# Kernel tuning notes

Hardware: AMD Instinct MI355X
Metric: run time of the kernel (lower is better)

## Reference

```python
import jax, jax.numpy as jnp
import numpy as np

NP, NM = 50, 32          # pathways, misc tokens
T = NP + NM              # 82 total tokens
D = 24                   # token_dim for latent_dim=2048: (2048//82)//4*4
H, DH, FF = 4, 6, 96     # heads, head_dim, ffn dim (4*D)
B = 8192
EPS = 1e-5


def _ln(x, g, b):
    m = x.mean(-1, keepdims=True)
    v = ((x - m) ** 2).mean(-1, keepdims=True)
    return (x - m) / jnp.sqrt(v + EPS) * g + b


def _adapter(x, w1, b1, g1, bb1, w2, b2, g2, bb2, w3, b3):
    # Linear -> LN -> GELU -> (Dropout eval) -> Linear -> LN -> GELU -> Linear
    h = jax.nn.gelu(_ln(x @ w1.T + b1, g1, bb1), approximate=False)
    h = jax.nn.gelu(_ln(h @ w2.T + b2, g2, bb2), approximate=False)
    return h @ w3.T + b3


def _enc_layer(x, wqkv, bqkv, wo, bo, lg1, lb1, fw1, fb1, fw2, fb2, lg2, lb2):
    # post-norm TransformerEncoderLayer (PyTorch defaults: relu FFN, batch_first)
    Bx, Tx, Dx = x.shape
    qkv = x @ wqkv.T + bqkv                       # [B,T,3D]
    q, k, v = jnp.split(qkv, 3, axis=-1)
    sh = lambda a: a.reshape(Bx, Tx, H, DH).transpose(0, 2, 1, 3)
    q, k, v = sh(q), sh(k), sh(v)
    att = jax.nn.softmax(jnp.einsum('bhqd,bhkd->bhqk', q, k) / jnp.sqrt(jnp.float32(DH)), axis=-1)
    o = jnp.einsum('bhqk,bhkd->bhqd', att, v).transpose(0, 2, 1, 3).reshape(Bx, Tx, Dx)
    o = o @ wo.T + bo
    x = _ln(x + o, lg1, lb1)
    f = jax.nn.relu(x @ fw1.T + fb1) @ fw2.T + fb2
    return _ln(x + f, lg2, lb2)


def setup_inputs() -> dict:
    key = jax.random.key(0)
    ks = iter(jax.random.split(key, 40))
    r = lambda *s: jax.random.normal(next(ks), s, dtype=jnp.float32) * 0.02
    inp = {
        'gene': jax.random.normal(next(ks), (B, 5000), dtype=jnp.float32),
        'protein': jax.random.normal(next(ks), (B, 226), dtype=jnp.float32),
        'pathway_tokens': jax.random.normal(next(ks), (NP, D), dtype=jnp.float32),
        'misc_tokens': jax.random.normal(next(ks), (NM, D), dtype=jnp.float32),
        # gene adapter: 5000 -> 512 -> 256 -> 82
        'gw1': r(512, 5000), 'gb1': jnp.zeros(512), 'gg1': jnp.ones(512), 'gbb1': jnp.zeros(512),
        'gw2': r(256, 512), 'gb2': jnp.zeros(256), 'gg2': jnp.ones(256), 'gbb2': jnp.zeros(256),
        'gw3': r(T, 256), 'gb3': jnp.zeros(T),
        # protein adapter: 226 -> 512 -> 256 -> 82
        'pw1': r(512, 226), 'pb1': jnp.zeros(512), 'pg1': jnp.ones(512), 'pbb1': jnp.zeros(512),
        'pw2': r(256, 512), 'pb2': jnp.zeros(256), 'pg2': jnp.ones(256), 'pbb2': jnp.zeros(256),
        'pw3': r(T, 256), 'pb3': jnp.zeros(T),
        # token mixer: 2 stacked TransformerEncoder layers
        'wqkv': r(2, 3 * D, D), 'bqkv': jnp.zeros((2, 3 * D)),
        'wo': r(2, D, D), 'bo': jnp.zeros((2, D)),
        'lg1': jnp.ones((2, D)), 'lb1': jnp.zeros((2, D)),
        'fw1': r(2, FF, D), 'fb1': jnp.zeros((2, FF)),
        'fw2': r(2, D, FF), 'fb2': jnp.zeros((2, D)),
        'lg2': jnp.ones((2, D)), 'lb2': jnp.zeros((2, D)),
    }
    return inp


def reference(gene, protein, pathway_tokens, misc_tokens,
              gw1, gb1, gg1, gbb1, gw2, gb2, gg2, gbb2, gw3, gb3,
              pw1, pb1, pg1, pbb1, pw2, pb2, pg2, pbb2, pw3, pb3,
              wqkv, bqkv, wo, bo, lg1, lb1, fw1, fb1, fw2, fb2, lg2, lb2):
    all_tokens = jnp.concatenate([pathway_tokens, misc_tokens], axis=0)    # [T,D]
    gene_w = jax.nn.softmax(_adapter(gene, gw1, gb1, gg1, gbb1, gw2, gb2, gg2, gbb2, gw3, gb3), axis=-1)
    prot_w = jax.nn.softmax(_adapter(protein, pw1, pb1, pg1, pbb1, pw2, pb2, pg2, pbb2, pw3, pb3), axis=-1)
    # vectorized form of the per-batch loop: token_activations[b] += all_tokens * w[b,:,None]
    acts = (gene_w + prot_w)[:, :, None] * all_tokens[None]               # [B,T,D]
    for l in range(2):
        acts = _enc_layer(acts, wqkv[l], bqkv[l], wo[l], bo[l], lg1[l], lb1[l],
                          fw1[l], fb1[l], fw2[l], fb2[l], lg2[l], lb2[l])
    return acts
```

## Files before the change

### kernel.cpp

```cpp
#include <hip/hip_runtime.h>
#include <hip/hip_bf16.h>
#include <math.h>

typedef __attribute__((ext_vector_type(4))) float f32x4;
typedef __attribute__((ext_vector_type(8))) short s16x8;
typedef __attribute__((ext_vector_type(4))) short s16x4;
typedef __attribute__((ext_vector_type(4))) unsigned int u32x4;
typedef __attribute__((ext_vector_type(2))) unsigned int u32x2;
typedef _Float16 h2 __attribute__((ext_vector_type(2)));

static __device__ __forceinline__ unsigned short f2bf(float f) {
  unsigned int u = __builtin_bit_cast(unsigned int, f);
  u += 0x7FFFu + ((u >> 16) & 1u);
  return (unsigned short)(u >> 16);
}
static __device__ __forceinline__ unsigned int pk2bf(float a, float b) {
  return (unsigned int)f2bf(a) | ((unsigned int)f2bf(b) << 16);
}
static __device__ __forceinline__ float gelu_exact(float x) {
  return 0.5f * x * (1.0f + erff(x * 0.7071067811865475f));
}
static __device__ __forceinline__ h2 pkh2(float a, float b) {
#if __has_builtin(__builtin_amdgcn_cvt_pkrtz)
  return __builtin_bit_cast(h2, __builtin_amdgcn_cvt_pkrtz(a, b));
#else
  h2 r; r[0] = (_Float16)a; r[1] = (_Float16)b; return r;
#endif
}
static __device__ __forceinline__ float dot2u(h2 a, unsigned int b, float c) {
  h2 bh = __builtin_bit_cast(h2, b);
#if __has_builtin(__builtin_amdgcn_fdot2)
  return __builtin_amdgcn_fdot2(a, bh, c, false);
#else
  return fmaf((float)a[0], (float)bh[0], fmaf((float)a[1], (float)bh[1], c));
#endif
}
static __device__ __forceinline__ float exp2fast(float x) {
#if __has_builtin(__builtin_amdgcn_exp2f)
  return __builtin_amdgcn_exp2f(x);
#else
  return exp2f(x);
#endif
}
static __device__ __forceinline__ void gll16(const void* g, void* l) {
#if __has_builtin(__builtin_amdgcn_global_load_lds)
  __builtin_amdgcn_global_load_lds((__attribute__((address_space(1))) void*)(void*)g,
                                   (__attribute__((address_space(3))) void*)l, 16, 0, 0);
#else
  *(u32x4*)l = *(const u32x4*)g;
#endif
}


__global__ __launch_bounds__(256)
void convert_tile_kernel(const float* __restrict__ src, unsigned short* __restrict__ dst,
                         int Msrc, int Ksrc, int TK, int total16) {
  const int id = blockIdx.x * 256 + threadIdx.x;
  if (id >= total16) return;
  const int j = id & 511;
  const int tile = id >> 9;
  const int tk = tile % TK;
  const int tmm = tile / TK;
  const int r = j >> 3, cb = j & 7;
  const int lcb = cb ^ (r & 7);
  const int row = tmm * 64 + r;
  const int col = tk * 64 + lcb * 8;
  float v[8];
  #pragma unroll
  for (int i = 0; i < 8; ++i) v[i] = 0.f;
  if (row < Msrc) {
    const size_t base = (size_t)row * Ksrc + col;
    if (col + 8 <= Ksrc && ((base & 3) == 0)) {
      f32x4 a = *(const f32x4*)(src + base);
      f32x4 b = *(const f32x4*)(src + base + 4);
      v[0]=a[0];v[1]=a[1];v[2]=a[2];v[3]=a[3];
      v[4]=b[0];v[5]=b[1];v[6]=b[2];v[7]=b[3];
    } else {
      #pragma unroll
      for (int i = 0; i < 8; ++i) if (col + i < Ksrc) v[i] = src[base + i];
    }
  }
  u32x4 o = { pk2bf(v[0],v[1]), pk2bf(v[2],v[3]), pk2bf(v[4],v[5]), pk2bf(v[6],v[7]) };
  *(u32x4*)(dst + (size_t)id * 8) = o;
}

__global__ __launch_bounds__(256, 4)
void gemm_bf16t_kernel(const unsigned short* __restrict__ At, const unsigned short* __restrict__ Bt,
                       const float* __restrict__ bias, float* __restrict__ C,
                       int NT, int KT, int Ntrue, int Nld) {
  __shared__ unsigned short As[4096];
  __shared__ unsigned short Bs[8192];
  const int tid = threadIdx.x;
  const int lane = tid & 63;
  const int wid = tid >> 6;
  const int wm = wid >> 1, wn = wid & 1;
  const int lr = lane & 15;
  const int lkb = ((lane >> 4) & 3) * 16;
  const int l = blockIdx.x;
  const int xcd = l & 7;
  const int kl = l >> 3;
  const int nb = kl % NT;
  const int tm = (kl / NT) * 8 + xcd;
  const size_t abase = (size_t)tm * KT * 4096;
  const size_t bbase0 = (size_t)(2 * nb) * KT * 4096;
  const size_t bbase1 = (size_t)(2 * nb + 1) * KT * 4096;

  f32x4 acc[2][4];
  #pragma unroll
  for (int m = 0; m < 2; ++m)
    #pragma unroll
    for (int n = 0; n < 4; ++n) acc[m][n] = (f32x4){0.f,0.f,0.f,0.f};

  for (int tk = 0; tk < KT; ++tk) {
    __syncthreads();
    const unsigned short* at = At + abase + (size_t)tk * 4096;
    const unsigned short* b0 = Bt + bbase0 + (size_t)tk * 4096;
    const unsigned short* b1 = Bt + bbase1 + (size_t)tk * 4096;
    gll16(at + tid * 8,        (char*)As + tid * 16);
    gll16(at + 2048 + tid * 8, (char*)As + 4096 + tid * 16);
    gll16(b0 + tid * 8,        (char*)Bs + tid * 16);
    gll16(b0 + 2048 + tid * 8, (char*)Bs + 4096 + tid * 16);
    gll16(b1 + tid * 8,        (char*)Bs + 8192 + tid * 16);
    gll16(b1 + 2048 + tid * 8, (char*)Bs + 12288 + tid * 16);
    __syncthreads();
    #pragma unroll
    for (int kk = 0; kk < 2; ++kk) {
      const int kb = (kk * 64 + lkb) ^ ((lr & 7) << 4);
      s16x8 af[2], bfr[4];
      #pragma unroll
      for (int m = 0; m < 2; ++m) {
        const int r = wm * 32 + m * 16 + lr;
        af[m] = *(const s16x8*)((const char*)As + r * 128 + kb);
      }
      #pragma unroll
      for (int n = 0; n < 4; ++n) {
        const int c = wn * 64 + n * 16 + lr;
        bfr[n] = *(const s16x8*)((const char*)Bs + (c >> 6) * 8192 + (c & 63) * 128 + kb);
      }
      #pragma unroll
      for (int m = 0; m < 2; ++m)
        #pragma unroll
        for (int n = 0; n < 4; ++n)
          acc[m][n] = __builtin_amdgcn_mfma_f32_16x16x32_bf16(af[m], bfr[n], acc[m][n], 0, 0, 0);
    }
  }
  const int crow = (lane >> 4) * 4;
  #pragma unroll
  for (int m = 0; m < 2; ++m) {
    const int row = tm * 64 + wm * 32 + m * 16 + crow;
    #pragma unroll
    for (int n = 0; n < 4; ++n) {
      const int col = nb * 128 + wn * 64 + n * 16 + lr;
      if (col < Ntrue) {
        const float bv = bias[col];
        #pragma unroll
        for (int i = 0; i < 4; ++i)
          C[(size_t)(row + i) * Nld + col] = acc[m][n][i] + bv;
      }
    }
  }
}

__global__ __launch_bounds__(256)
void ln_gelu_b16t_kernel(const float* __restrict__ X, const float* __restrict__ g,
                         const float* __restrict__ bta, unsigned short* __restrict__ Y,
                         int N, int TK) {
  const int lane = threadIdx.x & 63;
  const int row = blockIdx.x * 4 + (threadIdx.x >> 6);
  const int tmv = row >> 6, r = row & 63;
  const float* xr = X + (size_t)row * N;
  if (N == 512) {
    const int c0 = lane * 8;
    f32x4 a = *(const f32x4*)(xr + c0);
    f32x4 b = *(const f32x4*)(xr + c0 + 4);
    float s = a[0]+a[1]+a[2]+a[3]+b[0]+b[1]+b[2]+b[3];
    float ss = a[0]*a[0]+a[1]*a[1]+a[2]*a[2]+a[3]*a[3]+b[0]*b[0]+b[1]*b[1]+b[2]*b[2]+b[3]*b[3];
    #pragma unroll
    for (int off = 1; off < 64; off <<= 1) { s += __shfl_xor(s, off); ss += __shfl_xor(ss, off); }
    const float mean = s * (1.f/512.f);
    const float var = ss * (1.f/512.f) - mean * mean;
    const float rstd = rsqrtf(var + 1e-5f);
    float z[8];
    #pragma unroll
    for (int i = 0; i < 4; ++i) z[i]   = gelu_exact((a[i]-mean)*rstd*g[c0+i]   + bta[c0+i]);
    #pragma unroll
    for (int i = 0; i < 4; ++i) z[4+i] = gelu_exact((b[i]-mean)*rstd*g[c0+4+i] + bta[c0+4+i]);
    const int tk = lane >> 3, lcb = lane & 7;
    const size_t d16 = ((size_t)(tmv * TK + tk) << 9) + (r << 3) + (lcb ^ (r & 7));
    u32x4 o = { pk2bf(z[0],z[1]), pk2bf(z[2],z[3]), pk2bf(z[4],z[5]), pk2bf(z[6],z[7]) };
    *(u32x4*)(Y + d16 * 8) = o;
  } else {
    const int c0 = lane * 4;
    f32x4 a = *(const f32x4*)(xr + c0);
    float s = a[0]+a[1]+a[2]+a[3];
    float ss = a[0]*a[0]+a[1]*a[1]+a[2]*a[2]+a[3]*a[3];
    #pragma unroll
    for (int off = 1; off < 64; off <<= 1) { s += __shfl_xor(s, off); ss += __shfl_xor(ss, off); }
    const float mean = s * (1.f/256.f);
    const float var = ss * (1.f/256.f) - mean * mean;
    const float rstd = rsqrtf(var + 1e-5f);
    float z[4];
    #pragma unroll
    for (int i = 0; i < 4; ++i) z[i] = gelu_exact((a[i]-mean)*rstd*g[c0+i] + bta[c0+i]);
    const int tk = lane >> 4, lcb = (lane >> 1) & 7, half = lane & 1;
    const size_t d16 = ((size_t)(tmv * TK + tk) << 9) + (r << 3) + (lcb ^ (r & 7));
    u32x2 o = { pk2bf(z[0],z[1]), pk2bf(z[2],z[3]) };
    *(u32x2*)(Y + d16 * 8 + half * 4) = o;
  }
}

#define GBM 64
#define GBN 128
#define GBK 64
#define GLDS 72

__global__ __launch_bounds__(256, 2)
void gemm_bias_kernel(const float* __restrict__ A, const float* __restrict__ Bw,
                      const float* __restrict__ bias, float* __restrict__ C,
                      int M, int N, int K) {
  __shared__ short As[GBM * GLDS];
  __shared__ short Bs[GBN * GLDS];
  const int tid = threadIdx.x;
  const int lane = tid & 63;
  const int wid = tid >> 6;
  const int wm = wid >> 1;
  const int wn = wid & 1;
  const int m0 = blockIdx.x * GBM;
  const int n0 = blockIdx.y * GBN;
  const int lr = lane & 15;
  const int lk = (lane >> 4) * 8;
  const bool kAligned = ((K & 3) == 0);
  f32x4 acc[2][4];
  #pragma unroll
  for (int i = 0; i < 2; ++i)
    #pragma unroll
    for (int j = 0; j < 4; ++j) acc[i][j] = (f32x4){0.f, 0.f, 0.f, 0.f};
  for (int k0 = 0; k0 < K; k0 += GBK) {
    __syncthreads();
    const bool fullK = kAligned && (k0 + GBK <= K);
    #pragma unroll
    for (int pass = 0; pass < 4; ++pass) {
      const int f = pass * 1024 + tid * 4;
      const int r = f >> 6, c = f & 63;
      f32x4 v = (f32x4){0.f, 0.f, 0.f, 0.f};
      const float* src = A + (size_t)(m0 + r) * K + (k0 + c);
      if (fullK) v = *(const f32x4*)src;
      else {
        #pragma unroll
        for (int i = 0; i < 4; ++i) if (k0 + c + i < K) v[i] = src[i];
      }
      s16x4 sv = { (short)f2bf(v[0]), (short)f2bf(v[1]), (short)f2bf(v[2]), (short)f2bf(v[3]) };
      *(s16x4*)&As[r * GLDS + c] = sv;
    }
    #pragma unroll
    for (int pass = 0; pass < 8; ++pass) {
      const int f = pass * 1024 + tid * 4;
      const int r = f >> 6, c = f & 63;
      f32x4 v = (f32x4){0.f, 0.f, 0.f, 0.f};
      if (n0 + r < N) {
        const float* src = Bw + (size_t)(n0 + r) * K + (k0 + c);
        if (fullK) v = *(const f32x4*)src;
        else {
          #pragma unroll
          for (int i = 0; i < 4; ++i) if (k0 + c + i < K) v[i] = src[i];
        }
      }
      s16x4 sv = { (short)f2bf(v[0]), (short)f2bf(v[1]), (short)f2bf(v[2]), (short)f2bf(v[3]) };
      *(s16x4*)&Bs[r * GLDS + c] = sv;
    }
    __syncthreads();
    #pragma unroll
    for (int kk = 0; kk < GBK; kk += 32) {
      s16x8 af[2], bfr[4];
      #pragma unroll
      for (int m = 0; m < 2; ++m)
        af[m] = *(const s16x8*)&As[(wm * 32 + m * 16 + lr) * GLDS + kk + lk];
      #pragma unroll
      for (int n = 0; n < 4; ++n)
        bfr[n] = *(const s16x8*)&Bs[(wn * 64 + n * 16 + lr) * GLDS + kk + lk];
      #pragma unroll
      for (int m = 0; m < 2; ++m)
        #pragma unroll
        for (int n = 0; n < 4; ++n)
          acc[m][n] = __builtin_amdgcn_mfma_f32_16x16x32_bf16(af[m], bfr[n], acc[m][n], 0, 0, 0);
    }
  }
  const int crow = (lane >> 4) * 4;
  #pragma unroll
  for (int m = 0; m < 2; ++m) {
    const int row = m0 + wm * 32 + m * 16 + crow;
    #pragma unroll
    for (int n = 0; n < 4; ++n) {
      const int col = n0 + wn * 64 + n * 16 + lr;
      if (col < N) {
        const float bv = bias[col];
        #pragma unroll
        for (int i = 0; i < 4; ++i)
          C[(size_t)(row + i) * N + col] = acc[m][n][i] + bv;
      }
    }
  }
}

__global__ __launch_bounds__(256)
void ln_gelu_kernel(const float* __restrict__ X, const float* __restrict__ g,
                    const float* __restrict__ bta, float* __restrict__ Y, int N) {
  const int row = blockIdx.x;
  const float* xr = X + (size_t)row * N;
  float* yr = Y + (size_t)row * N;
  const int tid = threadIdx.x;
  const float e0 = xr[tid];
  float e1 = 0.f;
  const bool two = (N > 256);
  if (two) e1 = xr[tid + 256];
  float s = e0 + e1;
  float ss = e0 * e0 + e1 * e1;
  #pragma unroll
  for (int off = 1; off < 64; off <<= 1) { s += __shfl_xor(s, off); ss += __shfl_xor(ss, off); }
  __shared__ float red[8];
  const int w = tid >> 6;
  if ((tid & 63) == 0) { red[w] = s; red[4 + w] = ss; }
  __syncthreads();
  s  = red[0] + red[1] + red[2] + red[3];
  ss = red[4] + red[5] + red[6] + red[7];
  const float invN = 1.0f / (float)N;
  const float mean = s * invN;
  const float var = ss * invN - mean * mean;
  const float rstd = rsqrtf(var + 1e-5f);
  { const float z = (e0 - mean) * rstd * g[tid] + bta[tid]; yr[tid] = gelu_exact(z); }
  if (two) { const float z = (e1 - mean) * rstd * g[tid + 256] + bta[tid + 256]; yr[tid + 256] = gelu_exact(z); }
}

__global__ __launch_bounds__(256)
void softmax2_kernel(const float* __restrict__ la, const float* __restrict__ lp,
                     float* __restrict__ w, int B) {
  const int wid = threadIdx.x >> 6;
  const int lane = threadIdx.x & 63;
  const int row = blockIdx.x * 4 + wid;
  if (row >= B) return;
  const bool has2 = (lane < 18);
  const float* a = la + (size_t)row * 82;
  const float* p = lp + (size_t)row * 82;
  float a0 = a[lane], a1 = has2 ? a[64 + lane] : -1e30f;
  float m = fmaxf(a0, a1);
  #pragma unroll
  for (int off = 1; off < 64; off <<= 1) m = fmaxf(m, __shfl_xor(m, off));
  float ea0 = __expf(a0 - m);
  float ea1 = has2 ? __expf(a1 - m) : 0.f;
  float sa = ea0 + ea1;
  #pragma unroll
  for (int off = 1; off < 64; off <<= 1) sa += __shfl_xor(sa, off);
  float p0 = p[lane], p1 = has2 ? p[64 + lane] : -1e30f;
  float mp = fmaxf(p0, p1);
  #pragma unroll
  for (int off = 1; off < 64; off <<= 1) mp = fmaxf(mp, __shfl_xor(mp, off));
  float ep0 = __expf(p0 - mp);
  float ep1 = has2 ? __expf(p1 - mp) : 0.f;
  float sp = ep0 + ep1;
  #pragma unroll
  for (int off = 1; off < 64; off <<= 1) sp += __shfl_xor(sp, off);
  const float ia = 1.0f / sa, ip = 1.0f / sp;
  w[(size_t)row * 82 + lane] = ea0 * ia + ep0 * ip;
  if (has2) w[(size_t)row * 82 + 64 + lane] = ea1 * ia + ep1 * ip;
}

__global__ __launch_bounds__(256)
void pack_weights_kernel(const float* __restrict__ wqkv, const float* __restrict__ wo,
                         const float* __restrict__ fw1, const float* __restrict__ fw2,
                         unsigned int* __restrict__ dst) {
  const int i = blockIdx.x * 256 + threadIdx.x;
  if (i >= 6912) return;
  float a, b;
  if (i < 1728)      { a = wqkv[2 * i];            b = wqkv[2 * i + 1]; }
  else if (i < 2304) { int j = i - 1728; a = wo[2 * j];  b = wo[2 * j + 1]; }
  else if (i < 4608) { int j = i - 2304; a = fw1[2 * j]; b = fw1[2 * j + 1]; }
  else {
    int j = i - 4608; int layer = j / 1152; int r = j % 1152;
    int jp = r / 24; int d = r % 24;
    const float* s = fw2 + layer * 2304 + d * 96 + 2 * jp;
    a = s[0]; b = s[1];
  }
  unsigned short lo = __builtin_bit_cast(unsigned short, (_Float16)a);
  unsigned short hi = __builtin_bit_cast(unsigned short, (_Float16)b);
  dst[i] = (unsigned int)lo | ((unsigned int)hi << 16);
}

#define VSTRIDE 28

__global__ __launch_bounds__(256, 4)
void encoder_kernel(const float* __restrict__ w_sum,
                    const float* __restrict__ pathway, const float* __restrict__ misc,
                    const unsigned int* __restrict__ whb,
                    const float* __restrict__ bqkv, const float* __restrict__ bo,
                    const float* __restrict__ lg1, const float* __restrict__ lb1,
                    const float* __restrict__ fb1, const float* __restrict__ fb2,
                    const float* __restrict__ lg2, const float* __restrict__ lb2,
                    float* __restrict__ out, int Btot) {
  __shared__ unsigned int Ks[247 * 12];
  __shared__ unsigned int Vs[124 * VSTRIDE];
  const int tid = threadIdx.x;
  const bool active = (tid < 246);
  const int rowW = active ? tid : 246;
  int ls = tid / 82; if (ls > 2) ls = 2;
  const int t = active ? (tid - ls * 82) : 0;
  const int vrow = active ? (ls * 41 + (t >> 1)) : 123;
  const int b = blockIdx.x * 3 + ls;
  const bool storeOK = active && (b < Btot);
  const int bb = (b < Btot) ? b : (Btot - 1);
  float x[24];
  {
    const float* trow = (t < 50) ? (pathway + t * 24) : (misc + (t - 50) * 24);
    const float wv = w_sum[(size_t)bb * 82 + t];
    #pragma unroll
    for (int i = 0; i < 6; ++i) {
      f32x4 v = *(const f32x4*)(trow + 4 * i);
      x[4*i+0] = wv * v[0]; x[4*i+1] = wv * v[1];
      x[4*i+2] = wv * v[2]; x[4*i+3] = wv * v[3];
    }
  }
  const float QS = 0.5889777913f;
  float xf[24];
  #pragma unroll 1
  for (int layer = 0; layer < 2; ++layer) {
    const unsigned int* Wqh = whb + layer * 864;
    const unsigned int* Woh = whb + 1728 + layer * 288;
    const unsigned int* F1h = whb + 2304 + layer * 1152;
    const unsigned int* F2t = whb + 4608 + layer * 1152;
    const float* Bq = bqkv + layer * 72;
    h2 xh[12];
    #pragma unroll
    for (int i = 0; i < 12; ++i) xh[i] = pkh2(x[2*i], x[2*i+1]);
    h2 qh[12];
    #pragma unroll
    for (int j2 = 0; j2 < 12; ++j2) {
      float s0 = Bq[2*j2], s1 = Bq[2*j2+1];
      const unsigned int* w0 = Wqh + (2*j2) * 12;
      #pragma unroll
      for (int kd = 0; kd < 12; ++kd) { s0 = dot2u(xh[kd], w0[kd], s0); s1 = dot2u(xh[kd], w0[12 + kd], s1); }
      qh[j2] = pkh2(s0 * QS, s1 * QS);
    }
    {
      unsigned int kpk[12];
      #pragma unroll
      for (int j2 = 0; j2 < 12; ++j2) {
        float s0 = Bq[24 + 2*j2], s1 = Bq[25 + 2*j2];
        const unsigned int* w0 = Wqh + (24 + 2*j2) * 12;
        #pragma unroll
        for (int kd = 0; kd < 12; ++kd) { s0 = dot2u(xh[kd], w0[kd], s0); s1 = dot2u(xh[kd], w0[12 + kd], s1); }
        kpk[j2] = __builtin_bit_cast(unsigned int, pkh2(s0, s1));
      }
      #pragma unroll
      for (int u = 0; u < 3; ++u)
        *(u32x4*)&Ks[rowW * 12 + 4*u] = (u32x4){kpk[4*u], kpk[4*u+1], kpk[4*u+2], kpk[4*u+3]};
      float vv[24];
      #pragma unroll
      for (int j2 = 0; j2 < 12; ++j2) {
        float s0 = Bq[48 + 2*j2], s1 = Bq[49 + 2*j2];
        const unsigned int* w0 = Wqh + (48 + 2*j2) * 12;
        #pragma unroll
        for (int kd = 0; kd < 12; ++kd) { s0 = dot2u(xh[kd], w0[kd], s0); s1 = dot2u(xh[kd], w0[12 + kd], s1); }
        vv[2*j2] = s0; vv[2*j2+1] = s1;
      }
      _Float16* vh = (_Float16*)Vs;
      const int vbase = vrow * (2 * VSTRIDE) + (t & 1);
      #pragma unroll
      for (int j = 0; j < 24; ++j) vh[vbase + 2*j] = (_Float16)vv[j];
    }
    __syncthreads();
    float acc_o[24];
    float lsum[4] = {0.f, 0.f, 0.f, 0.f};
    #pragma unroll
// ... 88 lines not shown
      float sa = Bf1[2*jp], sb = Bf1[2*jp+1];
      const unsigned int* w1 = F1h + (2*jp) * 12;
      #pragma unroll
      for (int kd = 0; kd < 12; ++kd) { sa = dot2u(xnh[kd], w1[kd], sa); sb = dot2u(xnh[kd], w1[12 + kd], sb); }
      sa = fmaxf(sa, 0.f);
      sb = fmaxf(sb, 0.f);
      h2 sp = pkh2(sa, sb);
      const unsigned int* w2 = F2t + jp * 24;
      #pragma unroll
      for (int d = 0; d < 24; ++d) y[d] = dot2u(sp, w2[d], y[d]);
    }
    float mean2 = 0.f;
    #pragma unroll
    for (int j = 0; j < 24; ++j) mean2 += y[j];
    mean2 *= (1.f / 24.f);
    float var2 = 0.f;
    #pragma unroll
    for (int j = 0; j < 24; ++j) { const float dd = y[j] - mean2; var2 = fmaf(dd, dd, var2); }
    var2 *= (1.f / 24.f);
    const float rstd2 = rsqrtf(var2 + 1e-5f);
    const float* G2 = lg2 + layer * 24;
    const float* Bl2 = lb2 + layer * 24;
    #pragma unroll
    for (int j = 0; j < 24; ++j) xf[j] = (y[j] - mean2) * rstd2 * G2[j] + Bl2[j];
    if (layer == 0) {
      #pragma unroll
      for (int j = 0; j < 24; ++j) x[j] = xf[j];
    }
    __syncthreads();
  }
  if (storeOK) {
    float* op = out + (size_t)b * 1968 + t * 24;
    #pragma unroll
    for (int d4 = 0; d4 < 6; ++d4) {
      f32x4 v = { xf[4*d4], xf[4*d4+1], xf[4*d4+2], xf[4*d4+3] };
      *(f32x4*)(op + 4 * d4) = v;
    }
  }
}

extern "C" void kernel_launch(void* const* d_in, const int* in_sizes, int n_in,
                              void* d_out, int out_size, void* d_ws, size_t ws_size,
                              hipStream_t stream) {
  const float* gene    = (const float*)d_in[0];
  const float* protein = (const float*)d_in[1];
  const float* pathway = (const float*)d_in[2];
  const float* misc    = (const float*)d_in[3];
  const float* gw1 = (const float*)d_in[4];
  const float* gb1 = (const float*)d_in[5];
  const float* gg1 = (const float*)d_in[6];
  const float* gbb1= (const float*)d_in[7];
  const float* gw2 = (const float*)d_in[8];
  const float* gb2 = (const float*)d_in[9];
  const float* gg2 = (const float*)d_in[10];
  const float* gbb2= (const float*)d_in[11];
  const float* gw3 = (const float*)d_in[12];
  const float* gb3 = (const float*)d_in[13];
  const float* pw1 = (const float*)d_in[14];
  const float* pb1 = (const float*)d_in[15];
  const float* pg1 = (const float*)d_in[16];
  const float* pbb1= (const float*)d_in[17];
  const float* pw2 = (const float*)d_in[18];
  const float* pb2 = (const float*)d_in[19];
  const float* pg2 = (const float*)d_in[20];
  const float* pbb2= (const float*)d_in[21];
  const float* pw3 = (const float*)d_in[22];
  const float* pb3 = (const float*)d_in[23];
  const float* wqkv= (const float*)d_in[24];
  const float* bqkv= (const float*)d_in[25];
  const float* wo  = (const float*)d_in[26];
  const float* bo  = (const float*)d_in[27];
  const float* lg1 = (const float*)d_in[28];
  const float* lb1 = (const float*)d_in[29];
  const float* fw1 = (const float*)d_in[30];
  const float* fb1 = (const float*)d_in[31];
  const float* fw2 = (const float*)d_in[32];
  const float* fb2 = (const float*)d_in[33];
  const float* lg2 = (const float*)d_in[34];
  const float* lb2 = (const float*)d_in[35];

  const int B = in_sizes[0] / 5000;
  dim3 blk(256);

  size_t off = 0;
  auto take = [&](size_t bytes) { size_t r = off; off = (off + bytes + 255) & ~(size_t)255; return r; };
  const size_t o_geneB  = take((size_t)B * 5056 * 2);
  const size_t o_protB  = take((size_t)B * 256 * 2);
  const size_t o_gw1B   = take((size_t)512 * 5056 * 2);
  const size_t o_pw1B   = take((size_t)512 * 256 * 2);
  const size_t o_gw2B   = take((size_t)256 * 512 * 2);
  const size_t o_pw2B   = take((size_t)256 * 512 * 2);
  const size_t o_gw3B   = take((size_t)128 * 256 * 2);
  const size_t o_pw3B   = take((size_t)128 * 256 * 2);
  const size_t o_Cbuf   = take((size_t)B * 512 * 4);
  const size_t o_h1B    = take((size_t)B * 512 * 2);
  const size_t o_h2B    = take((size_t)B * 256 * 2);
  const size_t o_lg     = take((size_t)B * 82 * 4);
  const size_t o_lp     = take((size_t)B * 82 * 4);
  const size_t o_wsum   = take((size_t)B * 82 * 4);
  const size_t o_whb    = take((size_t)6912 * 4);
  const size_t need = off;

  if (need <= ws_size) {
    char* base = (char*)d_ws;
    unsigned short* geneB = (unsigned short*)(base + o_geneB);
    unsigned short* protB = (unsigned short*)(base + o_protB);
    unsigned short* gw1B  = (unsigned short*)(base + o_gw1B);
    unsigned short* pw1B  = (unsigned short*)(base + o_pw1B);
    unsigned short* gw2B  = (unsigned short*)(base + o_gw2B);
    unsigned short* pw2B  = (unsigned short*)(base + o_pw2B);
    unsigned short* gw3B  = (unsigned short*)(base + o_gw3B);
    unsigned short* pw3B  = (unsigned short*)(base + o_pw3B);
    float* Cbuf = (float*)(base + o_Cbuf);
    unsigned short* h1B = (unsigned short*)(base + o_h1B);
    unsigned short* h2B = (unsigned short*)(base + o_h2B);
    float* logits_g = (float*)(base + o_lg);
    float* logits_p = (float*)(base + o_lp);
    float* w_sum    = (float*)(base + o_wsum);
    unsigned int* whb = (unsigned int*)(base + o_whb);

    const int MT = B / 64;
    pack_weights_kernel<<<dim3(27), blk, 0, stream>>>(wqkv, wo, fw1, fw2, whb);
    {
      int t16 = MT * 79 * 512;
      convert_tile_kernel<<<dim3((t16 + 255) / 256), blk, 0, stream>>>(gene, geneB, B, 5000, 79, t16);
      t16 = MT * 4 * 512;
      convert_tile_kernel<<<dim3((t16 + 255) / 256), blk, 0, stream>>>(protein, protB, B, 226, 4, t16);
      t16 = 8 * 79 * 512;
      convert_tile_kernel<<<dim3((t16 + 255) / 256), blk, 0, stream>>>(gw1, gw1B, 512, 5000, 79, t16);
      t16 = 8 * 4 * 512;
      convert_tile_kernel<<<dim3((t16 + 255) / 256), blk, 0, stream>>>(pw1, pw1B, 512, 226, 4, t16);
      t16 = 4 * 8 * 512;
      convert_tile_kernel<<<dim3((t16 + 255) / 256), blk, 0, stream>>>(gw2, gw2B, 256, 512, 8, t16);
      convert_tile_kernel<<<dim3((t16 + 255) / 256), blk, 0, stream>>>(pw2, pw2B, 256, 512, 8, t16);
      t16 = 2 * 4 * 512;
      convert_tile_kernel<<<dim3((t16 + 255) / 256), blk, 0, stream>>>(gw3, gw3B, 82, 256, 4, t16);
      convert_tile_kernel<<<dim3((t16 + 255) / 256), blk, 0, stream>>>(pw3, pw3B, 82, 256, 4, t16);
    }
    gemm_bf16t_kernel<<<dim3(MT * 4), blk, 0, stream>>>(geneB, gw1B, gb1, Cbuf, 4, 79, 512, 512);
    ln_gelu_b16t_kernel<<<dim3(B / 4), blk, 0, stream>>>(Cbuf, gg1, gbb1, h1B, 512, 8);
    gemm_bf16t_kernel<<<dim3(MT * 2), blk, 0, stream>>>(h1B, gw2B, gb2, Cbuf, 2, 8, 256, 256);
    ln_gelu_b16t_kernel<<<dim3(B / 4), blk, 0, stream>>>(Cbuf, gg2, gbb2, h2B, 256, 4);
    gemm_bf16t_kernel<<<dim3(MT * 1), blk, 0, stream>>>(h2B, gw3B, gb3, logits_g, 1, 4, 82, 82);
    gemm_bf16t_kernel<<<dim3(MT * 4), blk, 0, stream>>>(protB, pw1B, pb1, Cbuf, 4, 4, 512, 512);
    ln_gelu_b16t_kernel<<<dim3(B / 4), blk, 0, stream>>>(Cbuf, pg1, pbb1, h1B, 512, 8);
    gemm_bf16t_kernel<<<dim3(MT * 2), blk, 0, stream>>>(h1B, pw2B, pb2, Cbuf, 2, 8, 256, 256);
    ln_gelu_b16t_kernel<<<dim3(B / 4), blk, 0, stream>>>(Cbuf, pg2, pbb2, h2B, 256, 4);
    gemm_bf16t_kernel<<<dim3(MT * 1), blk, 0, stream>>>(h2B, pw3B, pb3, logits_p, 1, 4, 82, 82);
    softmax2_kernel<<<dim3((B + 3) / 4), blk, 0, stream>>>(logits_g, logits_p, w_sum, B);
    encoder_kernel<<<dim3((B + 2) / 3), blk, 0, stream>>>(w_sum, pathway, misc,
        whb, bqkv, bo, lg1, lb1, fb1, fb2, lg2, lb2, (float*)d_out, B);
    return;
  }

  float* bufA = (float*)d_ws;
  float* bufB = bufA + (size_t)B * 512;
  float* logits_g = bufB + (size_t)B * 512;
  float* logits_p = logits_g + (size_t)B * 82;
  float* w_sum    = logits_p + (size_t)B * 82;
  unsigned int* whb = (unsigned int*)(w_sum + (size_t)B * 82);

  pack_weights_kernel<<<dim3(27), blk, 0, stream>>>(wqkv, wo, fw1, fw2, whb);
  gemm_bias_kernel<<<dim3(B / 64, 4), blk, 0, stream>>>(gene, gw1, gb1, bufA, B, 512, 5000);
  ln_gelu_kernel<<<dim3(B), blk, 0, stream>>>(bufA, gg1, gbb1, bufB, 512);
  gemm_bias_kernel<<<dim3(B / 64, 2), blk, 0, stream>>>(bufB, gw2, gb2, bufA, B, 256, 512);
  ln_gelu_kernel<<<dim3(B), blk, 0, stream>>>(bufA, gg2, gbb2, bufB, 256);
  gemm_bias_kernel<<<dim3(B / 64, 1), blk, 0, stream>>>(bufB, gw3, gb3, logits_g, B, 82, 256);
  gemm_bias_kernel<<<dim3(B / 64, 4), blk, 0, stream>>>(protein, pw1, pb1, bufA, B, 512, 226);
  ln_gelu_kernel<<<dim3(B), blk, 0, stream>>>(bufA, pg1, pbb1, bufB, 512);
  gemm_bias_kernel<<<dim3(B / 64, 2), blk, 0, stream>>>(bufB, pw2, pb2, bufA, B, 256, 512);
  ln_gelu_kernel<<<dim3(B), blk, 0, stream>>>(bufA, pg2, pbb2, bufB, 256);
  gemm_bias_kernel<<<dim3(B / 64, 1), blk, 0, stream>>>(bufB, pw3, pb3, logits_p, B, 82, 256);
  softmax2_kernel<<<dim3((B + 3) / 4), blk, 0, stream>>>(logits_g, logits_p, w_sum, B);
  encoder_kernel<<<dim3((B + 2) / 3), blk, 0, stream>>>(w_sum, pathway, misc,
      whb, bqkv, bo, lg1, lb1, fb1, fb2, lg2, lb2, (float*)d_out, B);
}
```

Baseline: 559.9 us.

## Rewrite transformer encoder as per-wave MFMA kernel with bf16 LDS staging

Replaces the scalar/packed-dot encoder kernel with a new kernel where each wave processes one batch sample, computing QKV, attention scores, PV, output projection and the FFN with bf16 16x16x32 MFMA instructions on tokens padded to 96. Weights are converted to bf16 inside each block into about 134 KB of dynamic LDS, so the separate pack_weights launch is dropped. Softmax is folded in by using exp2 on scaled scores without max subtraction, and normalisation is applied after PV. This trades extra per-block weight conversion, one block per CU occupancy and bf16 rounding of intermediates for far fewer ALU instructions in the attention and FFN.

```diff
diff --git a/kernel.cpp b/kernel.cpp
--- a/kernel.cpp
+++ b/kernel.cpp
@@ -16,6 +16,9 @@
 }
 static __device__ __forceinline__ unsigned int pk2bf(float a, float b) {
   return (unsigned int)f2bf(a) | ((unsigned int)f2bf(b) << 16);
+}
+static __device__ __forceinline__ float bf2f(unsigned short u) {
+  return __builtin_bit_cast(float, (unsigned int)u << 16);
 }
 static __device__ __forceinline__ float gelu_exact(float x) {
   return 0.5f * x * (1.0f + erff(x * 0.7071067811865475f));
@@ -50,7 +53,6 @@
   *(u32x4*)l = *(const u32x4*)g;
 #endif
 }
-
 
 __global__ __launch_bounds__(256)
 void convert_tile_kernel(const float* __restrict__ src, unsigned short* __restrict__ dst,
@@ -134,8 +136,8 @@
       }
       #pragma unroll
       for (int n = 0; n < 4; ++n) {
-        const int c = wn * 64 + n * 16 + lr;
-        bfr[n] = *(const s16x8*)((const char*)Bs + (c >> 6) * 8192 + (c & 63) * 128 + kb);
+        const int cc = wn * 64 + n * 16 + lr;
+        bfr[n] = *(const s16x8*)((const char*)Bs + (cc >> 6) * 8192 + (cc & 63) * 128 + kb);
       }
       #pragma unroll
       for (int m = 0; m < 2; ++m)
@@ -206,6 +208,411 @@
     const size_t d16 = ((size_t)(tmv * TK + tk) << 9) + (r << 3) + (lcb ^ (r & 7));
     u32x2 o = { pk2bf(z[0],z[1]), pk2bf(z[2],z[3]) };
     *(u32x2*)(Y + d16 * 8 + half * 4) = o;
+  }
+}
+
+__global__ __launch_bounds__(256)
+void softmax2_kernel(const float* __restrict__ la, const float* __restrict__ lp,
+                     float* __restrict__ w, int B) {
+  const int wid = threadIdx.x >> 6;
+  const int lane = threadIdx.x & 63;
+  const int row = blockIdx.x * 4 + wid;
+  if (row >= B) return;
+  const bool has2 = (lane < 18);
+  const float* a = la + (size_t)row * 82;
+  const float* p = lp + (size_t)row * 82;
+  float a0 = a[lane], a1 = has2 ? a[64 + lane] : -1e30f;
+  float m = fmaxf(a0, a1);
+  #pragma unroll
+  for (int off = 1; off < 64; off <<= 1) m = fmaxf(m, __shfl_xor(m, off));
+  float ea0 = __expf(a0 - m);
+  float ea1 = has2 ? __expf(a1 - m) : 0.f;
+  float sa = ea0 + ea1;
+  #pragma unroll
+  for (int off = 1; off < 64; off <<= 1) sa += __shfl_xor(sa, off);
+  float p0 = p[lane], p1 = has2 ? p[64 + lane] : -1e30f;
+  float mp = fmaxf(p0, p1);
+  #pragma unroll
+  for (int off = 1; off < 64; off <<= 1) mp = fmaxf(mp, __shfl_xor(mp, off));
+  float ep0 = __expf(p0 - mp);
+  float ep1 = has2 ? __expf(p1 - mp) : 0.f;
+  float sp = ep0 + ep1;
+  #pragma unroll
+  for (int off = 1; off < 64; off <<= 1) sp += __shfl_xor(sp, off);
+  const float ia = 1.0f / sa, ip = 1.0f / sp;
+  w[(size_t)row * 82 + lane] = ea0 * ia + ep0 * ip;
+  if (has2) w[(size_t)row * 82 + 64 + lane] = ea1 * ia + ep1 * ip;
+}
+
+#define TSTR 40
+#define VSTR 104
+#define OFF_WQ 0
+#define OFF_WO 6400
+#define OFF_F1 8960
+#define OFF_F2 16640
+#define OFF_SA 23296
+#define OFF_SP 38656
+#define OFF_SV 54016
+#define LDS_SHORTS 67328
+
+static __device__ __forceinline__ s16x8 frag40(const unsigned short* buf, int rowBase, int lane) {
+  const int r = rowBase + (lane & 15);
+  return *(const s16x8*)(buf + r * TSTR + 8 * (lane >> 4));
+}
+static __device__ __forceinline__ s16x8 frag104(const unsigned short* buf, int rowBase, int kOff, int lane) {
+  const int r = rowBase + (lane & 15);
+  return *(const s16x8*)(buf + r * VSTR + kOff + 8 * (lane >> 4));
+}
+
+__global__ __launch_bounds__(256, 1)
+void encoder_mfma_kernel(const float* __restrict__ w_sum,
+                         const float* __restrict__ pathway, const float* __restrict__ misc,
+                         const float* __restrict__ wqkv, const float* __restrict__ bqkv,
+                         const float* __restrict__ wo, const float* __restrict__ bo,
+                         const float* __restrict__ lg1, const float* __restrict__ lb1,
+                         const float* __restrict__ fw1, const float* __restrict__ fb1,
+                         const float* __restrict__ fw2, const float* __restrict__ fb2,
+                         const float* __restrict__ lg2, const float* __restrict__ lb2,
+                         float* __restrict__ out, int Btot) {
+  extern __shared__ unsigned short lds[];
+  const int tid = threadIdx.x;
+  const int lane = tid & 63;
+  const int wv = tid >> 6;
+  const int g = lane >> 4;
+  const int c = lane & 15;
+  const int q4 = g * 4;
+
+  #pragma unroll
+  for (int l = 0; l < 2; ++l) {
+    for (int r = tid; r < 80; r += 256) {
+      unsigned short* dst = lds + OFF_WQ + l * 3200 + r * TSTR;
+      unsigned int d[12];
+      if (r < 72) {
+        const float* s = wqkv + l * 1728 + r * 24;
+        #pragma unroll
+        for (int k = 0; k < 12; ++k) d[k] = pk2bf(s[2*k], s[2*k+1]);
+      } else {
+        #pragma unroll
+        for (int k = 0; k < 12; ++k) d[k] = 0u;
+      }
+      *(u32x4*)(dst)      = (u32x4){d[0],d[1],d[2],d[3]};
+      *(u32x4*)(dst + 8)  = (u32x4){d[4],d[5],d[6],d[7]};
+      *(u32x4*)(dst + 16) = (u32x4){d[8],d[9],d[10],d[11]};
+      *(u32x4*)(dst + 24) = (u32x4){0,0,0,0};
+      *(u32x4*)(dst + 32) = (u32x4){0,0,0,0};
+    }
+    for (int r = tid; r < 32; r += 256) {
+      unsigned short* dst = lds + OFF_WO + l * 1280 + r * TSTR;
+      unsigned int d[12];
+      if (r < 24) {
+        const float* s = wo + l * 576 + r * 24;
+        #pragma unroll
+        for (int k = 0; k < 12; ++k) d[k] = pk2bf(s[2*k], s[2*k+1]);
+      } else {
+        #pragma unroll
+        for (int k = 0; k < 12; ++k) d[k] = 0u;
+      }
+      *(u32x4*)(dst)      = (u32x4){d[0],d[1],d[2],d[3]};
+      *(u32x4*)(dst + 8)  = (u32x4){d[4],d[5],d[6],d[7]};
+      *(u32x4*)(dst + 16) = (u32x4){d[8],d[9],d[10],d[11]};
+      *(u32x4*)(dst + 24) = (u32x4){0,0,0,0};
+      *(u32x4*)(dst + 32) = (u32x4){0,0,0,0};
+    }
+    for (int r = tid; r < 96; r += 256) {
+      unsigned short* dst = lds + OFF_F1 + l * 3840 + r * TSTR;
+      const float* s = fw1 + l * 2304 + r * 24;
+      unsigned int d[12];
+      #pragma unroll
+      for (int k = 0; k < 12; ++k) d[k] = pk2bf(s[2*k], s[2*k+1]);
+      *(u32x4*)(dst)      = (u32x4){d[0],d[1],d[2],d[3]};
+      *(u32x4*)(dst + 8)  = (u32x4){d[4],d[5],d[6],d[7]};
+      *(u32x4*)(dst + 16) = (u32x4){d[8],d[9],d[10],d[11]};
+      *(u32x4*)(dst + 24) = (u32x4){0,0,0,0};
+      *(u32x4*)(dst + 32) = (u32x4){0,0,0,0};
+    }
+    for (int r = tid; r < 32; r += 256) {
+      unsigned short* dst = lds + OFF_F2 + l * 3328 + r * VSTR;
+      if (r < 24) {
+        const float* s = fw2 + l * 2304 + r * 96;
+        #pragma unroll
+        for (int k4 = 0; k4 < 12; ++k4) {
+          u32x4 d = { pk2bf(s[8*k4],   s[8*k4+1]), pk2bf(s[8*k4+2], s[8*k4+3]),
+                      pk2bf(s[8*k4+4], s[8*k4+5]), pk2bf(s[8*k4+6], s[8*k4+7]) };
+          *(u32x4*)(dst + 8*k4) = d;
+        }
+      } else {
+        #pragma unroll
+        for (int k4 = 0; k4 < 12; ++k4) *(u32x4*)(dst + 8*k4) = (u32x4){0,0,0,0};
+      }
+      *(u32x4*)(dst + 96) = (u32x4){0,0,0,0};
+    }
+  }
+  __syncthreads();
+
+  unsigned short* SA = lds + OFF_SA + wv * 3840;
+  unsigned short* SP = lds + OFF_SP + wv * 3840;
+  unsigned short* SV = lds + OFF_SV + wv * 3328;
+  const int b = blockIdx.x * 4 + wv;
+  const int bb = (b < Btot) ? b : (Btot - 1);
+
+  for (int s = lane; s < 480; s += 64) ((u32x4*)SP)[s] = (u32x4){0,0,0,0};
+  for (int s = lane; s < 416; s += 64) ((u32x4*)SV)[s] = (u32x4){0,0,0,0};
+  for (int r = lane; r < 96; r += 64) {
+    unsigned short* dst = SA + r * TSTR;
+    if (r < 82) {
+      const float* trow = (r < 50) ? (pathway + r * 24) : (misc + (r - 50) * 24);
+      const float wvv = w_sum[(size_t)bb * 82 + r];
+      unsigned int d[12];
+      #pragma unroll
+      for (int k = 0; k < 6; ++k) {
+        f32x4 v = *(const f32x4*)(trow + 4 * k);
+        d[2*k]   = pk2bf(wvv * v[0], wvv * v[1]);
+        d[2*k+1] = pk2bf(wvv * v[2], wvv * v[3]);
+      }
+      *(u32x4*)(dst)      = (u32x4){d[0],d[1],d[2],d[3]};
+      *(u32x4*)(dst + 8)  = (u32x4){d[4],d[5],d[6],d[7]};
+      *(u32x4*)(dst + 16) = (u32x4){d[8],d[9],d[10],d[11]};
+    } else {
+      *(u32x4*)(dst)      = (u32x4){0,0,0,0};
+      *(u32x4*)(dst + 8)  = (u32x4){0,0,0,0};
+      *(u32x4*)(dst + 16) = (u32x4){0,0,0,0};
+    }
+    *(u32x4*)(dst + 24) = (u32x4){0,0,0,0};
+    *(u32x4*)(dst + 32) = (u32x4){0,0,0,0};
+  }
+
+  float xres[6][2][4];
+  #pragma unroll
+  for (int m = 0; m < 6; ++m)
+    #pragma unroll
+    for (int n = 0; n < 2; ++n)
+      #pragma unroll
+      for (int i = 0; i < 4; ++i)
+        xres[m][n][i] = bf2f(SA[(16*m + q4 + i) * TSTR + 16*n + c]);
+  s16x8 af[6];
+  #pragma unroll
+  for (int m = 0; m < 6; ++m) af[m] = frag40(SA, 16*m, lane);
+
+  const float QS = 0.5889777913f;
+  const f32x4 Z4 = (f32x4){0.f, 0.f, 0.f, 0.f};
+
+  #pragma unroll 1
+  for (int l = 0; l < 2; ++l) {
+    const unsigned short* Wq = lds + OFF_WQ + l * 3200;
+    const unsigned short* Wo = lds + OFF_WO + l * 1280;
+    const unsigned short* F1 = lds + OFF_F1 + l * 3840;
+    const unsigned short* F2 = lds + OFF_F2 + l * 3328;
+    const float* bqv = bqkv + l * 72;
+
+    #pragma unroll
+    for (int tn = 0; tn < 5; ++tn) {
+      s16x8 bq = frag40(Wq, 16 * tn, lane);
+      f32x4 a6[6];
+      #pragma unroll
+      for (int tm = 0; tm < 6; ++tm)
+        a6[tm] = __builtin_amdgcn_mfma_f32_16x16x32_bf16(af[tm], bq, Z4, 0, 0, 0);
+      const int j = tn * 16 + c;
+      const float bj = (j < 72) ? bqv[j] : 0.f;
+      #pragma unroll
+      for (int tm = 0; tm < 6; ++tm) {
+        const int tokb = 16 * tm + q4;
+        if (j < 24) {
+          #pragma unroll
+          for (int i = 0; i < 4; ++i)
+            SP[(tokb + i) * TSTR + j] = f2bf((a6[tm][i] + bj) * QS);
+        } else if (j < 48) {
+          #pragma unroll
+          for (int i = 0; i < 4; ++i)
+            SA[(tokb + i) * TSTR + (j - 24)] = f2bf(a6[tm][i] + bj);
+        } else if (j < 72) {
+          u32x2 w = { pk2bf(a6[tm][0] + bj, a6[tm][1] + bj),
+                      pk2bf(a6[tm][2] + bj, a6[tm][3] + bj) };
+          *(u32x2*)(SV + (j - 48) * VSTR + tokb) = w;
+        }
+      }
+    }
+    s16x8 qf[6];
+    #pragma unroll
+    for (int n = 0; n < 6; ++n) qf[n] = frag40(SP, 16*n, lane);
+
+    f32x4 ot[2][6];
+    #pragma unroll
+    for (int m = 0; m < 2; ++m)
+      #pragma unroll
+      for (int n = 0; n < 6; ++n) ot[m][n] = Z4;
+    float lsum[6] = {0.f, 0.f, 0.f, 0.f, 0.f, 0.f};
+    #pragma unroll
+    for (int p = 0; p < 3; ++p) {
+      s16x8 ka0 = frag40(SA, 32*p, lane);
+      s16x8 ka1 = frag40(SA, 32*p + 16, lane);
+      f32x4 st[2][6];
+      #pragma unroll
+      for (int n = 0; n < 6; ++n) {
+        st[0][n] = __builtin_amdgcn_mfma_f32_16x16x32_bf16(ka0, qf[n], Z4, 0, 0, 0);
+        st[1][n] = __builtin_amdgcn_mfma_f32_16x16x32_bf16(ka1, qf[n], Z4, 0, 0, 0);
+      }
+      #pragma unroll
+      for (int m = 0; m < 2; ++m)
+        #pragma unroll
+        for (int n = 0; n < 6; ++n) {
+          const int kbase = 32*p + 16*m + q4;
+          float pv[4];
+          #pragma unroll
+          for (int i = 0; i < 4; ++i) {
+            const float e = exp2fast(st[m][n][i]);
+            pv[i] = (kbase + i < 82) ? e : 0.f;
+            lsum[n] += pv[i];
+          }
+          u32x2 w = { pk2bf(pv[0], pv[1]), pk2bf(pv[2], pv[3]) };
+          *(u32x2*)(SP + (16*n + c) * TSTR + 16*m + q4) = w;
+        }
+      s16x8 va0 = frag104(SV, 0, 32*p, lane);
+      s16x8 va1 = frag104(SV, 16, 32*p, lane);
+      #pragma unroll
+      for (int n = 0; n < 6; ++n) {
+        s16x8 pf = frag40(SP, 16*n, lane);
+        ot[0][n] = __builtin_amdgcn_mfma_f32_16x16x32_bf16(va0, pf, ot[0][n], 0, 0, 0);
+        ot[1][n] = __builtin_amdgcn_mfma_f32_16x16x32_bf16(va1, pf, ot[1][n], 0, 0, 0);
+      }
+    }
+    #pragma unroll
+    for (int n = 0; n < 6; ++n) {
+      float lt = lsum[n];
+      lt += __shfl_xor(lt, 16);
+      lt += __shfl_xor(lt, 32);
+      const float inv = 1.0f / lt;
+      #pragma unroll
+      for (int m = 0; m < 2; ++m) {
+        f32x4 o = ot[m][n];
+        u32x2 w = { pk2bf(o[0]*inv, o[1]*inv), pk2bf(o[2]*inv, o[3]*inv) };
+        *(u32x2*)(SP + (16*n + c) * TSTR + 16*m + q4) = w;
+      }
+    }
+    s16x8 wof0 = frag40(Wo, 0, lane);
+    s16x8 wof1 = frag40(Wo, 16, lane);
+    const float bo0 = bo[l*24 + c];
+    const float bo1 = (c < 8) ? bo[l*24 + 16 + c] : 0.f;
+    const float g10 = lg1[l*24 + c];
+    const float g11 = (c < 8) ? lg1[l*24 + 16 + c] : 0.f;
+    const float be0 = lb1[l*24 + c];
+    const float be1 = (c < 8) ? lb1[l*24 + 16 + c] : 0.f;
+    float xn[6][2][4];
+    #pragma unroll
+    for (int m = 0; m < 6; ++m) {
+      s16x8 oa = frag40(SP, 16*m, lane);
+      f32x4 x0 = __builtin_amdgcn_mfma_f32_16x16x32_bf16(oa, wof0, Z4, 0, 0, 0);
+      f32x4 x1 = __builtin_amdgcn_mfma_f32_16x16x32_bf16(oa, wof1, Z4, 0, 0, 0);
+      #pragma unroll
+      for (int i = 0; i < 4; ++i) {
+        const float v0 = x0[i] + bo0 + xres[m][0][i];
+        const float v1 = ((c < 8) ? (x1[i] + bo1) : 0.f) + xres[m][1][i];
+        float s = v0 + v1;
+        s += __shfl_xor(s, 1); s += __shfl_xor(s, 2);
+        s += __shfl_xor(s, 4); s += __shfl_xor(s, 8);
+        const float mu = s * (1.f / 24.f);
+        const float d0 = v0 - mu;
+        const float d1 = (c < 8) ? (v1 - mu) : 0.f;
+        float vr = d0 * d0 + d1 * d1;
+        vr += __shfl_xor(vr, 1); vr += __shfl_xor(vr, 2);
+        vr += __shfl_xor(vr, 4); vr += __shfl_xor(vr, 8);
+        const float rstd = rsqrtf(vr * (1.f / 24.f) + 1e-5f);
+        xn[m][0][i] = d0 * rstd * g10 + be0;
+        xn[m][1][i] = (c < 8) ? (d1 * rstd * g11 + be1) : 0.f;
+      }
+    }
+    #pragma unroll
+    for (int m = 0; m < 6; ++m)
+      #pragma unroll
+      for (int n = 0; n < 2; ++n)
+        #pragma unroll
+        for (int i = 0; i < 4; ++i)
+          SP[(16*m + q4 + i) * TSTR + 16*n + c] = f2bf(xn[m][n][i]);
+    s16x8 xnb[6];
+    #pragma unroll
+    for (int n = 0; n < 6; ++n) xnb[n] = frag40(SP, 16*n, lane);
+    f32x4 ya[6][2];
+    #pragma unroll
+    for (int m = 0; m < 6; ++m) { ya[m][0] = Z4; ya[m][1] = Z4; }
+    const float* fb1v = fb1 + l * 96;
+    #pragma unroll
+    for (int hp = 0; hp < 3; ++hp) {
+      s16x8 f1a0 = frag40(F1, 32*hp, lane);
+      s16x8 f1a1 = frag40(F1, 32*hp + 16, lane);
+      #pragma unroll
+      for (int n = 0; n < 6; ++n) {
+        f32x4 h0 = __builtin_amdgcn_mfma_f32_16x16x32_bf16(f1a0, xnb[n], Z4, 0, 0, 0);
+        f32x4 h1 = __builtin_amdgcn_mfma_f32_16x16x32_bf16(f1a1, xnb[n], Z4, 0, 0, 0);
+        const int hb0 = 32*hp + q4, hb1 = 32*hp + 16 + q4;
+        float r0[4], r1[4];
+        #pragma unroll
+        for (int i = 0; i < 4; ++i) {
+          r0[i] = fmaxf(h0[i] + fb1v[hb0 + i], 0.f);
+          r1[i] = fmaxf(h1[i] + fb1v[hb1 + i], 0.f);
+        }
+        u32x2 w0 = { pk2bf(r0[0], r0[1]), pk2bf(r0[2], r0[3]) };
+        u32x2 w1 = { pk2bf(r1[0], r1[1]), pk2bf(r1[2], r1[3]) };
+        *(u32x2*)(SA + (16*n + c) * TSTR + q4) = w0;
+        *(u32x2*)(SA + (16*n + c) * TSTR + 16 + q4) = w1;
+      }
+      s16x8 f2f0 = frag104(F2, 0, 32*hp, lane);
+      s16x8 f2f1 = frag104(F2, 16, 32*hp, lane);
+      #pragma unroll
+      for (int m = 0; m < 6; ++m) {
+        s16x8 ha = frag40(SA, 16*m, lane);
+        ya[m][0] = __builtin_amdgcn_mfma_f32_16x16x32_bf16(ha, f2f0, ya[m][0], 0, 0, 0);
+        ya[m][1] = __builtin_amdgcn_mfma_f32_16x16x32_bf16(ha, f2f1, ya[m][1], 0, 0, 0);
+      }
+    }
+    const float fb20 = fb2[l*24 + c];
+    const float fb21 = (c < 8) ? fb2[l*24 + 16 + c] : 0.f;
+    const float g20 = lg2[l*24 + c];
+    const float g21 = (c < 8) ? lg2[l*24 + 16 + c] : 0.f;
+    const float be20 = lb2[l*24 + c];
+    const float be21 = (c < 8) ? lb2[l*24 + 16 + c] : 0.f;
+    float xf[6][2][4];
+    #pragma unroll
+    for (int m = 0; m < 6; ++m)
+      #pragma unroll
+      for (int i = 0; i < 4; ++i) {
+        const float v0 = ya[m][0][i] + fb20 + xn[m][0][i];
+        const float v1 = ((c < 8) ? (ya[m][1][i] + fb21) : 0.f) + xn[m][1][i];
+        float s = v0 + v1;
+        s += __shfl_xor(s, 1); s += __shfl_xor(s, 2);
+        s += __shfl_xor(s, 4); s += __shfl_xor(s, 8);
+        const float mu = s * (1.f / 24.f);
+        const float d0 = v0 - mu;
+        const float d1 = (c < 8) ? (v1 - mu) : 0.f;
+        float vr = d0 * d0 + d1 * d1;
+        vr += __shfl_xor(vr, 1); vr += __shfl_xor(vr, 2);
+        vr += __shfl_xor(vr, 4); vr += __shfl_xor(vr, 8);
+        const float rstd = rsqrtf(vr * (1.f / 24.f) + 1e-5f);
+        xf[m][0][i] = d0 * rstd * g20 + be20;
+        xf[m][1][i] = (c < 8) ? (d1 * rstd * g21 + be21) : 0.f;
+      }
+    if (l == 0) {
+      #pragma unroll
+      for (int m = 0; m < 6; ++m)
+        #pragma unroll
+        for (int n = 0; n < 2; ++n)
+          #pragma unroll
+          for (int i = 0; i < 4; ++i) {
+            SA[(16*m + q4 + i) * TSTR + 16*n + c] = f2bf(xf[m][n][i]);
+            xres[m][n][i] = xf[m][n][i];
+          }
+      #pragma unroll
+      for (int m = 0; m < 6; ++m) af[m] = frag40(SA, 16*m, lane);
+    } else if (b < Btot) {
+      #pragma unroll
+      for (int m = 0; m < 6; ++m)
+        #pragma unroll
+        for (int i = 0; i < 4; ++i) {
+          const int q = 16*m + q4 + i;
+          if (q < 82) {
+            out[(size_t)b * 1968 + q * 24 + c] = xf[m][0][i];
+            if (c < 8) out[(size_t)b * 1968 + q * 24 + 16 + c] = xf[m][1][i];
+          }
+        }
+    }
   }
 }
 
@@ -241,40 +648,40 @@
     #pragma unroll
     for (int pass = 0; pass < 4; ++pass) {
       const int f = pass * 1024 + tid * 4;
-      const int r = f >> 6, c = f & 63;
+      const int r = f >> 6, cc = f & 63;
       f32x4 v = (f32x4){0.f, 0.f, 0.f, 0.f};
-      const float* src = A + (size_t)(m0 + r) * K + (k0 + c);
+      const float* src = A + (size_t)(m0 + r) * K + (k0 + cc);
       if (fullK) v = *(const f32x4*)src;
       else {
         #pragma unroll
-        for (int i = 0; i < 4; ++i) if (k0 + c + i < K) v[i] = src[i];
+        for (int i = 0; i < 4; ++i) if (k0 + cc + i < K) v[i] = src[i];
       }
       s16x4 sv = { (short)f2bf(v[0]), (short)f2bf(v[1]), (short)f2bf(v[2]), (short)f2bf(v[3]) };
-      *(s16x4*)&As[r * GLDS + c] = sv;
+      *(s16x4*)&As[r * GLDS + cc] = sv;
     }
     #pragma unroll
     for (int pass = 0; pass < 8; ++pass) {
       const int f = pass * 1024 + tid * 4;
-      const int r = f >> 6, c = f & 63;
+      const int r = f >> 6, cc = f & 63;
       f32x4 v = (f32x4){0.f, 0.f, 0.f, 0.f};
       if (n0 + r < N) {
-        const float* src = Bw + (size_t)(n0 + r) * K + (k0 + c);
+        const float* src = Bw + (size_t)(n0 + r) * K + (k0 + cc);
         if (fullK) v = *(const f32x4*)src;
         else {
           #pragma unroll
-          for (int i = 0; i < 4; ++i) if (k0 + c + i < K) v[i] = src[i];
+          for (int i = 0; i < 4; ++i) if (k0 + cc + i < K) v[i] = src[i];
         }
       }
       s16x4 sv = { (short)f2bf(v[0]), (short)f2bf(v[1]), (short)f2bf(v[2]), (short)f2bf(v[3]) };
-      *(s16x4*)&Bs[r * GLDS + c] = sv;
+      *(s16x4*)&Bs[r * GLDS + cc] = sv;
     }
     __syncthreads();
     #pragma unroll
     for (int kk = 0; kk < GBK; kk += 32) {
-      s16x8 af[2], bfr[4];
+      s16x8 af2[2], bfr[4];
       #pragma unroll
       for (int m = 0; m < 2; ++m)
-        af[m] = *(const s16x8*)&As[(wm * 32 + m * 16 + lr) * GLDS + kk + lk];
+        af2[m] = *(const s16x8*)&As[(wm * 32 + m * 16 + lr) * GLDS + kk + lk];
       #pragma unroll
       for (int n = 0; n < 4; ++n)
         bfr[n] = *(const s16x8*)&Bs[(wn * 64 + n * 16 + lr) * GLDS + kk + lk];
@@ -282,7 +689,7 @@
       for (int m = 0; m < 2; ++m)
         #pragma unroll
         for (int n = 0; n < 4; ++n)
-          acc[m][n] = __builtin_amdgcn_mfma_f32_16x16x32_bf16(af[m], bfr[n], acc[m][n], 0, 0, 0);
+          acc[m][n] = __builtin_amdgcn_mfma_f32_16x16x32_bf16(af2[m], bfr[n], acc[m][n], 0, 0, 0);
     }
   }
   const int crow = (lane >> 4) * 4;
@@ -329,39 +736,6 @@
   const float rstd = rsqrtf(var + 1e-5f);
   { const float z = (e0 - mean) * rstd * g[tid] + bta[tid]; yr[tid] = gelu_exact(z); }
   if (two) { const float z = (e1 - mean) * rstd * g[tid + 256] + bta[tid + 256]; yr[tid + 256] = gelu_exact(z); }
-}
-
-__global__ __launch_bounds__(256)
-void softmax2_kernel(const float* __restrict__ la, const float* __restrict__ lp,
-                     float* __restrict__ w, int B) {
-  const int wid = threadIdx.x >> 6;
-  const int lane = threadIdx.x & 63;
-  const int row = blockIdx.x * 4 + wid;
-  if (row >= B) return;
-  const bool has2 = (lane < 18);
-  const float* a = la + (size_t)row * 82;
-  const float* p = lp + (size_t)row * 82;
-  float a0 = a[lane], a1 = has2 ? a[64 + lane] : -1e30f;
-  float m = fmaxf(a0, a1);
-  #pragma unroll
-  for (int off = 1; off < 64; off <<= 1) m = fmaxf(m, __shfl_xor(m, off));
-  float ea0 = __expf(a0 - m);
-  float ea1 = has2 ? __expf(a1 - m) : 0.f;
-  float sa = ea0 + ea1;
-  #pragma unroll
-  for (int off = 1; off < 64; off <<= 1) sa += __shfl_xor(sa, off);
-  float p0 = p[lane], p1 = has2 ? p[64 + lane] : -1e30f;
-  float mp = fmaxf(p0, p1);
-  #pragma unroll
-  for (int off = 1; off < 64; off <<= 1) mp = fmaxf(mp, __shfl_xor(mp, off));
-  float ep0 = __expf(p0 - mp);
-  float ep1 = has2 ? __expf(p1 - mp) : 0.f;
-  float sp = ep0 + ep1;
-  #pragma unroll
-  for (int off = 1; off < 64; off <<= 1) sp += __shfl_xor(sp, off);
-  const float ia = 1.0f / sa, ip = 1.0f / sp;
-  w[(size_t)row * 82 + lane] = ea0 * ia + ep0 * ip;
-  if (has2) w[(size_t)row * 82 + 64 + lane] = ea1 * ia + ep1 * ip;
 }
 
 __global__ __launch_bounds__(256)
@@ -386,7 +760,6 @@
 }
 
 #define VSTRIDE 28
-
 __global__ __launch_bounds__(256, 4)
 void encoder_kernel(const float* __restrict__ w_sum,
                     const float* __restrict__ pathway, const float* __restrict__ misc,
@@ -641,6 +1014,14 @@
   const int B = in_sizes[0] / 5000;
   dim3 blk(256);
 
+  static int mfma_lds_ok = -1;
+  if (mfma_lds_ok < 0) {
+    hipError_t e = hipFuncSetAttribute((const void*)encoder_mfma_kernel,
+        hipFuncAttributeMaxDynamicSharedMemorySize, LDS_SHORTS * 2);
+    mfma_lds_ok = 1;
+    (void)e;
+  }
+
   size_t off = 0;
   auto take = [&](size_t bytes) { size_t r = off; off = (off + bytes + 255) & ~(size_t)255; return r; };
   const size_t o_geneB  = take((size_t)B * 5056 * 2);
@@ -676,10 +1057,8 @@
     float* logits_g = (float*)(base + o_lg);
     float* logits_p = (float*)(base + o_lp);
     float* w_sum    = (float*)(base + o_wsum);
-    unsigned int* whb = (unsigned int*)(base + o_whb);
 
     const int MT = B / 64;
-    pack_weights_kernel<<<dim3(27), blk, 0, stream>>>(wqkv, wo, fw1, fw2, whb);
     {
       int t16 = MT * 79 * 512;
       convert_tile_kernel<<<dim3((t16 + 255) / 256), blk, 0, stream>>>(gene, geneB, B, 5000, 79, t16);
@@ -707,8 +1086,9 @@
     ln_gelu_b16t_kernel<<<dim3(B / 4), blk, 0, stream>>>(Cbuf, pg2, pbb2, h2B, 256, 4);
     gemm_bf16t_kernel<<<dim3(MT * 1), blk, 0, stream>>>(h2B, pw3B, pb3, logits_p, 1, 4, 82, 82);
     softmax2_kernel<<<dim3((B + 3) / 4), blk, 0, stream>>>(logits_g, logits_p, w_sum, B);
-    encoder_kernel<<<dim3((B + 2) / 3), blk, 0, stream>>>(w_sum, pathway, misc,
-        whb, bqkv, bo, lg1, lb1, fb1, fb2, lg2, lb2, (float*)d_out, B);
+    encoder_mfma_kernel<<<dim3((B + 3) / 4), blk, LDS_SHORTS * 2, stream>>>(
+        w_sum, pathway, misc, wqkv, bqkv, wo, bo, lg1, lb1,
+        fw1, fb1, fw2, fb2, lg2, lb2, (float*)d_out, B);
     return;
   }
 
```

Result: slower. 613.6 us (+9.6%).
